# Optimization experiments

Hardware: AMD Instinct MI355X
Metric: run time of the kernel (lower is better)

The kernel has to match this reference:

```python
import jax, jax.numpy as jnp
import numpy as np

B, N, C, H = 8, 1024, 384, 6
D = C // H
SPAN = C  # att_span = pos_ebd_size = dim (module sets max_relative_positions = dim)
SCALE_FACTOR = 3  # 1 + c2p + p2c


def setup_inputs() -> dict:
    key = jax.random.key(0)
    ks = jax.random.split(key, 10)
    w = lambda k, shp: jax.random.normal(k, shp, jnp.float32) * 0.02
    rel_pos = (jnp.arange(N)[:, None] - jnp.arange(N)[None, :]).astype(jnp.int32)
    return {
        "x": jax.random.normal(ks[0], (B, N, C), jnp.float32),
        "relative_pos": rel_pos,
        "rel_embeddings": jax.random.normal(ks[1], (2 * SPAN, C), jnp.float32) * 0.02,
        "Wq": w(ks[2], (C, C)), "bq": jnp.zeros((C,), jnp.float32),
        "Wk": w(ks[3], (C, C)), "bk": jnp.zeros((C,), jnp.float32),
        "Wv": w(ks[4], (C, C)), "bv": jnp.zeros((C,), jnp.float32),
        "Wpk": w(ks[5], (C, C)), "bpk": jnp.zeros((C,), jnp.float32),
        "Wpq": w(ks[6], (C, C)), "bpq": jnp.zeros((C,), jnp.float32),
        "Wo": w(ks[7], (C, C)), "bo": jnp.zeros((C,), jnp.float32),
    }


def reference(x, relative_pos, rel_embeddings, Wq, bq, Wk, bk, Wv, bv,
              Wpk, bpk, Wpq, bpq, Wo, bo):
    Bx, Nx, Cx = x.shape
    # content projections -> (B, H, N, D)
    q = (x @ Wq + bq).reshape(Bx, Nx, H, D).transpose(0, 2, 1, 3)
    k = (x @ Wk + bk).reshape(Bx, Nx, H, D).transpose(0, 2, 1, 3)
    v = (x @ Wv + bv).reshape(Bx, Nx, H, D).transpose(0, 2, 1, 3)
    scale = jnp.sqrt(jnp.asarray(D * SCALE_FACTOR, jnp.float32))
    attn = jnp.einsum('bhnd,bhmd->bhnm', q, k) / scale  # (B,H,N,N)

    # positional projections of rel_embeddings[0:2*SPAN] -> (H, 2*SPAN, D)
    pos_k = (rel_embeddings @ Wpk + bpk).reshape(2 * SPAN, H, D).transpose(1, 0, 2)
    pos_q = (rel_embeddings @ Wpq + bpq).reshape(2 * SPAN, H, D).transpose(1, 0, 2)

    rp = relative_pos.astype(jnp.int32)
    # content->position: gather columns of q @ pos_k^T by bucketed index
    c2p_pos = jnp.clip(rp + SPAN, 0, 2 * SPAN - 1)  # (N,N)
    c2p = jnp.einsum('bhnd,hpd->bhnp', q, pos_k)    # (B,H,N,2*SPAN)
    c2p = jnp.take_along_axis(
        c2p, jnp.broadcast_to(c2p_pos[None, None], (Bx, H, Nx, Nx)), axis=-1)

    # position->content: gather columns of k @ pos_q^T, then transpose
    p2c_pos = jnp.clip(-rp + SPAN, 0, 2 * SPAN - 1)
    p2c = jnp.einsum('bhnd,hpd->bhnp', k, pos_q)    # (B,H,N,2*SPAN)
    p2c = jnp.take_along_axis(
        p2c, jnp.broadcast_to(p2c_pos[None, None], (Bx, H, Nx, Nx)), axis=-1)
    p2c = jnp.swapaxes(p2c, -1, -2)

    attn = attn + (c2p + p2c) / scale
    probs = jax.nn.softmax(attn, axis=-1)
    out = jnp.einsum('bhnm,bhmd->bhnd', probs, v)
    out = out.transpose(0, 2, 1, 3).reshape(Bx, Nx, Cx)
    return out @ Wo + bo
```

## Files before the change

### kernel.cpp

```cpp
#include <hip/hip_runtime.h>
#include <math.h>

typedef __attribute__((ext_vector_type(8))) short short8;
typedef __attribute__((ext_vector_type(4))) float v4f;
typedef __attribute__((ext_vector_type(4))) unsigned short us4;

#define INV_SCALE 0.07216878364870322f

__device__ __forceinline__ unsigned short f2bf(float f) {
  unsigned u = __builtin_bit_cast(unsigned, f);
  u = (u + 0x7FFFu + ((u >> 16) & 1u)) >> 16;
  return (unsigned short)u;
}
__device__ __forceinline__ float bf2f(unsigned short h) {
  unsigned u = ((unsigned)h) << 16;
  return __builtin_bit_cast(float, u);
}

enum { OM_PLAIN = 0, OM_Q = 1, OM_K = 2, OM_VT = 3, OM_PK = 4, OM_PQ = 5 };

__global__ __launch_bounds__(256) void transpose_w(
    const float* __restrict__ Wq, const float* __restrict__ Wk,
    const float* __restrict__ Wv, const float* __restrict__ Wpk,
    const float* __restrict__ Wpq, const float* __restrict__ Wo,
    unsigned short* __restrict__ Wt) {
  __shared__ unsigned short Ts[64][68];
  const int mat = blockIdx.y;
  const float* W = mat == 0 ? Wq : mat == 1 ? Wk : mat == 2 ? Wv
                 : mat == 3 ? Wpk : mat == 4 ? Wpq : Wo;
  const int tk = (blockIdx.x % 6) * 64, tn = (blockIdx.x / 6) * 64;
  const int t = threadIdx.x;
#pragma unroll
  for (int it = 0; it < 4; ++it) {
    int r = (t >> 4) + it * 16, c = (t & 15) * 4;
    float4 v = *(const float4*)(W + (size_t)(tk + r) * 384 + tn + c);
    us4 p = {f2bf(v.x), f2bf(v.y), f2bf(v.z), f2bf(v.w)};
    *(us4*)&Ts[r][c] = p;
  }
  __syncthreads();
  unsigned short* out = Wt + (size_t)mat * 147456;
#pragma unroll
  for (int it = 0; it < 2; ++it) {
    int n = (t >> 3) + it * 32, kc = (t & 7) * 8;
    unsigned short tmp[8];
#pragma unroll
    for (int j = 0; j < 8; ++j) tmp[j] = Ts[kc + j][n];
    *(short8*)(out + (size_t)(tn + n) * 384 + tk + kc) = *(short8*)tmp;
  }
}

template <typename AT, int OMODE>
__device__ __forceinline__ void pgemm_body(
    const AT* __restrict__ A, const unsigned short* __restrict__ Bt,
    const float* __restrict__ bias, void* __restrict__ out,
    int m0, int n0, float scale, unsigned short (*Bs)[392]) {
  const int t = threadIdx.x;
  const int lane = t & 63, w = t >> 6, li = lane & 15, quad = lane >> 4;

  {
    int r = t >> 2, cq = (t & 3) * 96;
#pragma unroll
    for (int i = 0; i < 12; ++i)
      *(short8*)&Bs[r][cq + i * 8] =
          *(const short8*)(Bt + (size_t)(n0 + r) * 384 + cq + i * 8);
  }
  const int row = m0 + w * 16 + li;
  short8 afr[12];
#pragma unroll
  for (int kk = 0; kk < 12; ++kk) {
    if constexpr (sizeof(AT) == 4) {
      float4 u0 = *(const float4*)((const float*)A + (size_t)row * 384 + kk * 32 + quad * 8);
      float4 u1 = *(const float4*)((const float*)A + (size_t)row * 384 + kk * 32 + quad * 8 + 4);
      short8 v;
      v[0] = (short)f2bf(u0.x); v[1] = (short)f2bf(u0.y);
      v[2] = (short)f2bf(u0.z); v[3] = (short)f2bf(u0.w);
      v[4] = (short)f2bf(u1.x); v[5] = (short)f2bf(u1.y);
      v[6] = (short)f2bf(u1.z); v[7] = (short)f2bf(u1.w);
      afr[kk] = v;
    } else {
      afr[kk] = *(const short8*)((const unsigned short*)A + (size_t)row * 384 + kk * 32 + quad * 8);
    }
  }
  __syncthreads();

  v4f acc[4] = {};
#pragma unroll
  for (int kk = 0; kk < 12; ++kk) {
#pragma unroll
    for (int nt = 0; nt < 4; ++nt) {
      short8 bf = *(const short8*)&Bs[nt * 16 + li][kk * 32 + quad * 8];
      acc[nt] = __builtin_amdgcn_mfma_f32_16x16x32_bf16(afr[kk], bf, acc[nt], 0, 0, 0);
    }
  }

#pragma unroll
  for (int nt = 0; nt < 4; ++nt) {
    int col = n0 + nt * 16 + li;
    float bv = bias[col];
    int h = col >> 6, d = col & 63;
#pragma unroll
    for (int i = 0; i < 4; ++i) {
      int orow = m0 + w * 16 + quad * 4 + i;
      float val = (acc[nt][i] + bv) * scale;
      if constexpr (OMODE == OM_PLAIN) {
        ((float*)out)[(size_t)orow * 384 + col] = val;
      } else if constexpr (OMODE == OM_Q || OMODE == OM_K) {
        int b = orow >> 10, n = orow & 1023;
        ((unsigned short*)out)[((size_t)(b * 6 + h) << 16) + (n << 6) + d] = f2bf(val);
      } else if constexpr (OMODE == OM_VT) {
        int b = orow >> 10, n = orow & 1023;
        ((unsigned short*)out)[((size_t)(b * 6 + h) << 16) + (d << 10) + n] = f2bf(val);
      } else {
        ((unsigned short*)out)[(size_t)h * 49152 + (size_t)orow * 64 + d] = f2bf(val);
      }
    }
  }
}

__global__ __launch_bounds__(256, 3) void proj_all(
    const float* __restrict__ x, const float* __restrict__ re,
    const unsigned short* __restrict__ Wt,
    const float* __restrict__ bq, const float* __restrict__ bk,
    const float* __restrict__ bv, const float* __restrict__ bpk,
    const float* __restrict__ bpq,
    unsigned short* __restrict__ qw, unsigned short* __restrict__ kw,
    unsigned short* __restrict__ vtw, unsigned short* __restrict__ pkw,
    unsigned short* __restrict__ pqw) {
  __shared__ __align__(16) unsigned short Bs[64][392];
  const int which = blockIdx.y / 6;
  const int n0 = (blockIdx.y % 6) * 64;
  const int m0 = blockIdx.x * 64;
  if (which >= 3 && m0 >= 768) return;
  const float* A = which < 3 ? x : re;
  const unsigned short* Bt = Wt + (size_t)which * 147456;
  switch (which) {
    case 0: pgemm_body<float, OM_Q >(A, Bt, bq,  qw,  m0, n0, INV_SCALE, Bs); break;
    case 1: pgemm_body<float, OM_K >(A, Bt, bk,  kw,  m0, n0, 1.f, Bs); break;
    case 2: pgemm_body<float, OM_VT>(A, Bt, bv,  vtw, m0, n0, 1.f, Bs); break;
    case 3: pgemm_body<float, OM_PK>(A, Bt, bpk, pkw, m0, n0, 1.f, Bs); break;
    default: pgemm_body<float, OM_PQ>(A, Bt, bpq, pqw, m0, n0, INV_SCALE, Bs); break;
  }
}

__global__ __launch_bounds__(256, 3) void out_gemm(
    const unsigned short* __restrict__ ao, const unsigned short* __restrict__ Bt,
    const float* __restrict__ bo, float* __restrict__ out) {
  __shared__ __align__(16) unsigned short Bs[64][392];
  pgemm_body<unsigned short, OM_PLAIN>(ao, Bt, bo, out,
                                       blockIdx.x * 64, blockIdx.y * 64, 1.f, Bs);
}

#define ASTR 72

__global__ __launch_bounds__(256, 3) void attn_fused(
    const unsigned short* __restrict__ q, const unsigned short* __restrict__ k,
    const unsigned short* __restrict__ vt, const unsigned short* __restrict__ pk,
    const unsigned short* __restrict__ pq, unsigned short* __restrict__ ao) {
  __shared__ __align__(16) unsigned short band1[128][ASTR];
  __shared__ __align__(16) unsigned short band2[128][ASTR];
  __shared__ __align__(16) unsigned short Ps[64][ASTR];

  const int f = blockIdx.x + (blockIdx.y << 4);
  const int g = f & 7, s = f >> 3;
  const int bh = g * 6 + (s >> 4);
  const int n0 = (s & 15) * 64;
  const int h = bh % 6, b = bh / 6;
  const int t = threadIdx.x;
  const int lane = t & 63, w = t >> 6;
  const int li = lane & 15, quad = lane >> 4;

  const unsigned short* qb = q + ((size_t)bh << 16);
  const unsigned short* kb = k + ((size_t)bh << 16);
  const unsigned short* vb = vt + ((size_t)bh << 16);
  const unsigned short* pkh = pk + (size_t)h * 49152;
  const unsigned short* pqh = pq + (size_t)h * 49152;

  short8 aq0 = *(const short8*)(qb + (size_t)(n0 + w * 16 + li) * 64 + quad * 8);
  short8 aq1 = *(const short8*)(qb + (size_t)(n0 + w * 16 + li) * 64 + 32 + quad * 8);

  float l_part[4] = {0.f, 0.f, 0.f, 0.f};
  v4f o[4] = {};

  const int sr = t >> 1, sc = (t & 1) * 32;
  short8 st1[4], st2[4];
  {
    int src = n0 - 0 - 63 + 384 + sr;
    src = src < 0 ? 0 : (src > 767 ? 767 : src);
    const unsigned short* p1 = pkh + (size_t)src * 64 + sc;
    const unsigned short* p2 = pqh + (size_t)src * 64 + sc;
#pragma unroll
    for (int ss = 0; ss < 4; ++ss) {
      st1[ss] = *(const short8*)(p1 + ss * 8);
      st2[ss] = *(const short8*)(p2 + ss * 8);
    }
  }

  for (int j0 = 0; j0 < 1024; j0 += 64) {
    __syncthreads();
#pragma unroll
    for (int ss = 0; ss < 4; ++ss) {
      *(short8*)&band1[sr][sc + ss * 8] = st1[ss];
      *(short8*)&band2[sr][sc + ss * 8] = st2[ss];
    }
    __syncthreads();

    {
      int src = n0 - (j0 + 64) - 63 + 384 + sr;
      src = src < 0 ? 0 : (src > 767 ? 767 : src);
      const unsigned short* p1 = pkh + (size_t)src * 64 + sc;
      const unsigned short* p2 = pqh + (size_t)src * 64 + sc;
#pragma unroll
      for (int ss = 0; ss < 4; ++ss) {
        st1[ss] = *(const short8*)(p1 + ss * 8);
        st2[ss] = *(const short8*)(p2 + ss * 8);
      }
    }

    short8 ak0 = *(const short8*)(kb + (size_t)(j0 + w * 16 + li) * 64 + quad * 8);
    short8 ak1 = *(const short8*)(kb + (size_t)(j0 + w * 16 + li) * 64 + 32 + quad * 8);

    v4f t1a[8] = {}, t2a[8] = {};
#pragma unroll
    for (int ct = 0; ct < 8; ++ct) {
      short8 b10 = *(const short8*)&band1[ct * 16 + li][quad * 8];
      short8 b11 = *(const short8*)&band1[ct * 16 + li][32 + quad * 8];
      t1a[ct] = __builtin_amdgcn_mfma_f32_16x16x32_bf16(aq0, b10, t1a[ct], 0, 0, 0);
      t1a[ct] = __builtin_amdgcn_mfma_f32_16x16x32_bf16(aq1, b11, t1a[ct], 0, 0, 0);
      short8 b20 = *(const short8*)&band2[ct * 16 + li][quad * 8];
      short8 b21 = *(const short8*)&band2[ct * 16 + li][32 + quad * 8];
      t2a[ct] = __builtin_amdgcn_mfma_f32_16x16x32_bf16(ak0, b20, t2a[ct], 0, 0, 0);
      t2a[ct] = __builtin_amdgcn_mfma_f32_16x16x32_bf16(ak1, b21, t2a[ct], 0, 0, 0);
    }
    __syncthreads();

#pragma unroll
    for (int ct = 0; ct < 8; ++ct) {
      us4 p1 = {f2bf(t1a[ct][0]), f2bf(t1a[ct][1]), f2bf(t1a[ct][2]), f2bf(t1a[ct][3])};
      us4 p2 = {f2bf(t2a[ct][0]), f2bf(t2a[ct][1]), f2bf(t2a[ct][2]), f2bf(t2a[ct][3])};
      *(us4*)&band1[ct * 16 + li][w * 16 + quad * 4] = p1;
      *(us4*)&band2[ct * 16 + li][w * 16 + quad * 4] = p2;
    }
    v4f sqk[4] = {};
#pragma unroll
    for (int nt = 0; nt < 4; ++nt) {
      short8 b0 = *(const short8*)(kb + (size_t)(j0 + nt * 16 + li) * 64 + quad * 8);
      short8 b1 = *(const short8*)(kb + (size_t)(j0 + nt * 16 + li) * 64 + 32 + quad * 8);
      sqk[nt] = __builtin_amdgcn_mfma_f32_16x16x32_bf16(aq0, b0, sqk[nt], 0, 0, 0);
      sqk[nt] = __builtin_amdgcn_mfma_f32_16x16x32_bf16(aq1, b1, sqk[nt], 0, 0, 0);
    }
    __syncthreads();

#pragma unroll
    for (int nt = 0; nt < 4; ++nt) {
      int jl = nt * 16 + li;
#pragma unroll
      for (int i = 0; i < 4; ++i) {
        int nl = w * 16 + quad * 4 + i;
        int r = nl - jl + 63;
        float s2 = sqk[nt][i] + bf2f(band1[r][nl]) + bf2f(band2[r][jl]);
        float p = __expf(s2);
        l_part[i] += p;
        Ps[nl][jl] = f2bf(p);
      }
    }
#pragma unroll
    for (int kst = 0; kst < 2; ++kst) {
      short8 ap = *(const short8*)&Ps[w * 16 + li][kst * 32 + quad * 8];
#pragma unroll
      for (int nt = 0; nt < 4; ++nt) {
        short8 bv2 = *(const short8*)(vb + (size_t)(nt * 16 + li) * 1024 + j0 + kst * 32 + quad * 8);
        o[nt] = __builtin_amdgcn_mfma_f32_16x16x32_bf16(ap, bv2, o[nt], 0, 0, 0);
      }
    }
  }

#pragma unroll
  for (int i = 0; i < 4; ++i) {
    float l = l_part[i];
    l += __shfl_xor(l, 1);
    l += __shfl_xor(l, 2);
    l += __shfl_xor(l, 4);
    l += __shfl_xor(l, 8);
    float inv_l = 1.f / l;
    int nl = w * 16 + quad * 4 + i;
#pragma unroll
    for (int nt = 0; nt < 4; ++nt)
      ao[((size_t)(b * 1024 + n0 + nl)) * 384 + h * 64 + nt * 16 + li] =
          f2bf(o[nt][i] * inv_l);
  }
}

extern "C" void kernel_launch(void* const* d_in, const int* in_sizes, int n_in,
                              void* d_out, int out_size, void* d_ws,
                              size_t ws_size, hipStream_t stream) {
  const float* x   = (const float*)d_in[0];
  const float* re  = (const float*)d_in[2];
  const float* Wq  = (const float*)d_in[3];
  const float* bq  = (const float*)d_in[4];
  const float* Wk  = (const float*)d_in[5];
  const float* bk  = (const float*)d_in[6];
  const float* Wv  = (const float*)d_in[7];
  const float* bv  = (const float*)d_in[8];
  const float* Wpk = (const float*)d_in[9];
  const float* bpk = (const float*)d_in[10];
  const float* Wpq = (const float*)d_in[11];
  const float* bpq = (const float*)d_in[12];
  const float* Wo  = (const float*)d_in[13];
  const float* bo  = (const float*)d_in[14];
  float* out = (float*)d_out;

  unsigned short* ws = (unsigned short*)d_ws;
  unsigned short* Wt  = ws;
  unsigned short* qw  = Wt + 884736;
  unsigned short* kw  = qw + 3145728;
  unsigned short* vtw = kw + 3145728;
  unsigned short* pkw = vtw + 3145728;
  unsigned short* pqw = pkw + 294912;
  unsigned short* aow = pqw + 294912;

  transpose_w<<<dim3(36, 6), 256, 0, stream>>>(Wq, Wk, Wv, Wpk, Wpq, Wo, Wt);
  proj_all<<<dim3(128, 30), 256, 0, stream>>>(x, re, Wt, bq, bk, bv, bpk, bpq,
                                              qw, kw, vtw, pkw, pqw);
  attn_fused<<<dim3(16, 48), 256, 0, stream>>>(qw, kw, vtw, pkw, pqw, aow);
  out_gemm<<<dim3(128, 6), 256, 0, stream>>>(aow, Wt + 5 * 147456, bo, out);
}
```

Before: 271.6 us.

## Pre-convert activations to bf16 and reuse A fragments across three N tiles

Adds a kernel that converts x and rel_embeddings to bf16 once. The projection and output GEMMs now keep the A-row fragments in registers and loop over three 64-column weight tiles per block. This removes the repeated fp32 loads and conversions of A, which previously happened once per N tile. In exchange there is an extra launch and an extra workspace round trip, fewer blocks (10 rows instead of 30 for proj, 2 instead of 6 for out), and the weight-tile reload between passes is serialized.

```diff
diff --git a/kernel.cpp b/kernel.cpp
--- a/kernel.cpp
+++ b/kernel.cpp
@@ -18,6 +18,29 @@
 }
 
 enum { OM_PLAIN = 0, OM_Q = 1, OM_K = 2, OM_VT = 3, OM_PK = 4, OM_PQ = 5 };
+
+__global__ __launch_bounds__(256) void cvt_bf16(
+    const float* __restrict__ x, const float* __restrict__ re,
+    unsigned short* __restrict__ xb, unsigned short* __restrict__ reb) {
+  size_t idx = ((size_t)blockIdx.x * 256 + threadIdx.x) * 8;
+  const float* src;
+  unsigned short* dst;
+  if (idx < 3145728) {
+    src = x + idx; dst = xb + idx;
+  } else {
+    size_t r = idx - 3145728;
+    if (r >= 294912) return;
+    src = re + r; dst = reb + r;
+  }
+  float4 u0 = *(const float4*)src;
+  float4 u1 = *(const float4*)(src + 4);
+  short8 v;
+  v[0] = (short)f2bf(u0.x); v[1] = (short)f2bf(u0.y);
+  v[2] = (short)f2bf(u0.z); v[3] = (short)f2bf(u0.w);
+  v[4] = (short)f2bf(u1.x); v[5] = (short)f2bf(u1.y);
+  v[6] = (short)f2bf(u1.z); v[7] = (short)f2bf(u1.w);
+  *(short8*)dst = v;
+}
 
 __global__ __launch_bounds__(256) void transpose_w(
     const float* __restrict__ Wq, const float* __restrict__ Wk,
@@ -49,76 +72,73 @@
   }
 }
 
-template <typename AT, int OMODE>
+template <int OMODE, int NP>
 __device__ __forceinline__ void pgemm_body(
-    const AT* __restrict__ A, const unsigned short* __restrict__ Bt,
+    const unsigned short* __restrict__ A, const unsigned short* __restrict__ Bt,
     const float* __restrict__ bias, void* __restrict__ out,
-    int m0, int n0, float scale, unsigned short (*Bs)[392]) {
+    int m0, int ng0, float scale, unsigned short (*Bs)[392]) {
   const int t = threadIdx.x;
   const int lane = t & 63, w = t >> 6, li = lane & 15, quad = lane >> 4;
-
-  {
-    int r = t >> 2, cq = (t & 3) * 96;
-#pragma unroll
-    for (int i = 0; i < 12; ++i)
-      *(short8*)&Bs[r][cq + i * 8] =
-          *(const short8*)(Bt + (size_t)(n0 + r) * 384 + cq + i * 8);
-  }
   const int row = m0 + w * 16 + li;
+  const int sr = t >> 2, scq = (t & 3) * 96;
+
+#pragma unroll
+  for (int i = 0; i < 12; ++i)
+    *(short8*)&Bs[sr][scq + i * 8] =
+        *(const short8*)(Bt + (size_t)(ng0 * 64 + sr) * 384 + scq + i * 8);
+
   short8 afr[12];
 #pragma unroll
-  for (int kk = 0; kk < 12; ++kk) {
-    if constexpr (sizeof(AT) == 4) {
-      float4 u0 = *(const float4*)((const float*)A + (size_t)row * 384 + kk * 32 + quad * 8);
-      float4 u1 = *(const float4*)((const float*)A + (size_t)row * 384 + kk * 32 + quad * 8 + 4);
-      short8 v;
-      v[0] = (short)f2bf(u0.x); v[1] = (short)f2bf(u0.y);
-      v[2] = (short)f2bf(u0.z); v[3] = (short)f2bf(u0.w);
-      v[4] = (short)f2bf(u1.x); v[5] = (short)f2bf(u1.y);
-      v[6] = (short)f2bf(u1.z); v[7] = (short)f2bf(u1.w);
-      afr[kk] = v;
-    } else {
-      afr[kk] = *(const short8*)((const unsigned short*)A + (size_t)row * 384 + kk * 32 + quad * 8);
-    }
-  }
-  __syncthreads();
-
-  v4f acc[4] = {};
-#pragma unroll
-  for (int kk = 0; kk < 12; ++kk) {
+  for (int kk = 0; kk < 12; ++kk)
+    afr[kk] = *(const short8*)(A + (size_t)row * 384 + kk * 32 + quad * 8);
+
+#pragma unroll
+  for (int pp = 0; pp < NP; ++pp) {
+    __syncthreads();
+    v4f acc[4] = {};
+#pragma unroll
+    for (int kk = 0; kk < 12; ++kk) {
+#pragma unroll
+      for (int nt = 0; nt < 4; ++nt) {
+        short8 bf = *(const short8*)&Bs[nt * 16 + li][kk * 32 + quad * 8];
+        acc[nt] = __builtin_amdgcn_mfma_f32_16x16x32_bf16(afr[kk], bf, acc[nt], 0, 0, 0);
+      }
+    }
+    __syncthreads();
+    if (pp + 1 < NP) {
+#pragma unroll
+      for (int i = 0; i < 12; ++i)
+        *(short8*)&Bs[sr][scq + i * 8] =
+            *(const short8*)(Bt + (size_t)((ng0 + pp + 1) * 64 + sr) * 384 + scq + i * 8);
+    }
+    const int n0 = (ng0 + pp) * 64;
 #pragma unroll
     for (int nt = 0; nt < 4; ++nt) {
-      short8 bf = *(const short8*)&Bs[nt * 16 + li][kk * 32 + quad * 8];
-      acc[nt] = __builtin_amdgcn_mfma_f32_16x16x32_bf16(afr[kk], bf, acc[nt], 0, 0, 0);
-    }
-  }
-
-#pragma unroll
-  for (int nt = 0; nt < 4; ++nt) {
-    int col = n0 + nt * 16 + li;
-    float bv = bias[col];
-    int h = col >> 6, d = col & 63;
-#pragma unroll
-    for (int i = 0; i < 4; ++i) {
-      int orow = m0 + w * 16 + quad * 4 + i;
-      float val = (acc[nt][i] + bv) * scale;
-      if constexpr (OMODE == OM_PLAIN) {
-        ((float*)out)[(size_t)orow * 384 + col] = val;
-      } else if constexpr (OMODE == OM_Q || OMODE == OM_K) {
-        int b = orow >> 10, n = orow & 1023;
-        ((unsigned short*)out)[((size_t)(b * 6 + h) << 16) + (n << 6) + d] = f2bf(val);
-      } else if constexpr (OMODE == OM_VT) {
-        int b = orow >> 10, n = orow & 1023;
-        ((unsigned short*)out)[((size_t)(b * 6 + h) << 16) + (d << 10) + n] = f2bf(val);
-      } else {
-        ((unsigned short*)out)[(size_t)h * 49152 + (size_t)orow * 64 + d] = f2bf(val);
+      int col = n0 + nt * 16 + li;
+      float bv = bias[col];
+      int h = col >> 6, d = col & 63;
+#pragma unroll
+      for (int i = 0; i < 4; ++i) {
+        int orow = m0 + w * 16 + quad * 4 + i;
+        float val = (acc[nt][i] + bv) * scale;
+        if constexpr (OMODE == OM_PLAIN) {
+          ((float*)out)[(size_t)orow * 384 + col] = val;
+        } else if constexpr (OMODE == OM_Q || OMODE == OM_K) {
+          int b = orow >> 10, n = orow & 1023;
+          ((unsigned short*)out)[((size_t)(b * 6 + h) << 16) + (n << 6) + d] = f2bf(val);
+        } else if constexpr (OMODE == OM_VT) {
+          int b = orow >> 10, n = orow & 1023;
+          ((unsigned short*)out)[((size_t)(b * 6 + h) << 16) + (d << 10) + n] = f2bf(val);
+        } else {
+          ((unsigned short*)out)[(size_t)h * 49152 + (size_t)orow * 64 + d] = f2bf(val);
+        }
       }
     }
   }
 }
 
 __global__ __launch_bounds__(256, 3) void proj_all(
-    const float* __restrict__ x, const float* __restrict__ re,
+    const unsigned short* __restrict__ xb, const unsigned short* __restrict__ reb,
     const unsigned short* __restrict__ Wt,
     const float* __restrict__ bq, const float* __restrict__ bk,
     const float* __restrict__ bv, const float* __restrict__ bpk,
@@ -127,18 +147,24 @@
     unsigned short* __restrict__ vtw, unsigned short* __restrict__ pkw,
     unsigned short* __restrict__ pqw) {
   __shared__ __align__(16) unsigned short Bs[64][392];
-  const int which = blockIdx.y / 6;
-  const int n0 = (blockIdx.y % 6) * 64;
+  const int y = blockIdx.y;
   const int m0 = blockIdx.x * 64;
-  if (which >= 3 && m0 >= 768) return;
-  const float* A = which < 3 ? x : re;
+  int which, ng0;
+  if (y < 6) {
+    which = y >> 1; ng0 = (y & 1) * 3;
+  } else {
+    int p = y - 6;
+    which = 3 + (p >> 1); ng0 = (p & 1) * 3;
+    if (m0 >= 768) return;
+  }
+  const unsigned short* A = which < 3 ? xb : reb;
   const unsigned short* Bt = Wt + (size_t)which * 147456;
   switch (which) {
-    case 0: pgemm_body<float, OM_Q >(A, Bt, bq,  qw,  m0, n0, INV_SCALE, Bs); break;
-    case 1: pgemm_body<float, OM_K >(A, Bt, bk,  kw,  m0, n0, 1.f, Bs); break;
-    case 2: pgemm_body<float, OM_VT>(A, Bt, bv,  vtw, m0, n0, 1.f, Bs); break;
-    case 3: pgemm_body<float, OM_PK>(A, Bt, bpk, pkw, m0, n0, 1.f, Bs); break;
-    default: pgemm_body<float, OM_PQ>(A, Bt, bpq, pqw, m0, n0, INV_SCALE, Bs); break;
+    case 0: pgemm_body<OM_Q, 3>(A, Bt, bq,  qw,  m0, ng0, INV_SCALE, Bs); break;
+    case 1: pgemm_body<OM_K, 3>(A, Bt, bk,  kw,  m0, ng0, 1.f, Bs); break;
+    case 2: pgemm_body<OM_VT,3>(A, Bt, bv,  vtw, m0, ng0, 1.f, Bs); break;
+    case 3: pgemm_body<OM_PK,3>(A, Bt, bpk, pkw, m0, ng0, 1.f, Bs); break;
+    default: pgemm_body<OM_PQ,3>(A, Bt, bpq, pqw, m0, ng0, INV_SCALE, Bs); break;
   }
 }
 
@@ -146,8 +172,8 @@
     const unsigned short* __restrict__ ao, const unsigned short* __restrict__ Bt,
     const float* __restrict__ bo, float* __restrict__ out) {
   __shared__ __align__(16) unsigned short Bs[64][392];
-  pgemm_body<unsigned short, OM_PLAIN>(ao, Bt, bo, out,
-                                       blockIdx.x * 64, blockIdx.y * 64, 1.f, Bs);
+  pgemm_body<OM_PLAIN, 3>(ao, Bt, bo, out,
+                          blockIdx.x * 64, blockIdx.y * 3, 1.f, Bs);
 }
 
 #define ASTR 72
@@ -317,10 +343,13 @@
   unsigned short* pkw = vtw + 3145728;
   unsigned short* pqw = pkw + 294912;
   unsigned short* aow = pqw + 294912;
-
+  unsigned short* xb  = aow + 3145728;
+  unsigned short* reb = xb + 3145728;
+
+  cvt_bf16<<<dim3(1680), 256, 0, stream>>>(x, re, xb, reb);
   transpose_w<<<dim3(36, 6), 256, 0, stream>>>(Wq, Wk, Wv, Wpk, Wpq, Wo, Wt);
-  proj_all<<<dim3(128, 30), 256, 0, stream>>>(x, re, Wt, bq, bk, bv, bpk, bpq,
+  proj_all<<<dim3(128, 10), 256, 0, stream>>>(xb, reb, Wt, bq, bk, bv, bpk, bpq,
                                               qw, kw, vtw, pkw, pqw);
   attn_fused<<<dim3(16, 48), 256, 0, stream>>>(qw, kw, vtw, pkw, pqw, aow);
-  out_gemm<<<dim3(128, 6), 256, 0, stream>>>(aow, Wt + 5 * 147456, bo, out);
-}
+  out_gemm<<<dim3(128, 2), 256, 0, stream>>>(aow, Wt + 5 * 147456, bo, out);
+}
```

After: 260.4 us. -4.1%, faster.
